# Kernel tuning notes

Measured on AMD Instinct MI355X. Metric: run time of the kernel, lower is better.

## Reference

```python
import jax, jax.numpy as jnp
import numpy as np

NUM_HEADS = 16
ROTARY_BASE = 10000.0


def _apply_rotary(x):
    # x: (B, S, H, D); GPT-NeoX style rotate-half over full head dim
    B, S, H, D = x.shape
    half = D // 2
    inv_freq = 1.0 / (ROTARY_BASE ** (jnp.arange(0, half, dtype=jnp.float32) / half))
    t = jnp.arange(S, dtype=jnp.float32)
    freqs = jnp.einsum('s,d->sd', t, inv_freq)          # (S, half)
    cos = jnp.cos(freqs)[None, :, None, :]               # (1, S, 1, half)
    sin = jnp.sin(freqs)[None, :, None, :]
    x1, x2 = x[..., :half], x[..., half:]
    return jnp.concatenate([x1 * cos - x2 * sin, x2 * cos + x1 * sin], axis=-1).astype(x.dtype)


def setup_inputs() -> dict:
    key = jax.random.key(0)
    k0, k1, k2 = jax.random.split(key, 3)
    B, S, E = 2, 2048, 2048
    x = jax.random.normal(k0, (B, S, E), dtype=jnp.float32)
    wqkv = jax.random.normal(k1, (3 * E, E), dtype=jnp.float32) * 0.02
    bqkv = jnp.zeros((3 * E,), dtype=jnp.float32)
    wout = jax.random.normal(k2, (E, E), dtype=jnp.float32) * 0.02
    bout = jnp.zeros((E,), dtype=jnp.float32)
    return {"x": x, "wqkv": wqkv, "bqkv": bqkv, "wout": wout, "bout": bout}


def reference(x, wqkv, bqkv, wout, bout):
    B, S, E = x.shape
    H = NUM_HEADS
    D = E // H
    # fused QKV projection: (B, S, 3, H, D)
    qkv = (jnp.einsum('bse,fe->bsf', x, wqkv) + bqkv).reshape(B, S, 3, H, D)
    q, k, v = qkv[:, :, 0], qkv[:, :, 1], qkv[:, :, 2]
    q = _apply_rotary(q)
    k = _apply_rotary(k)
    scale = 1.0 / jnp.sqrt(jnp.float32(D))
    scores = jnp.einsum('bthd,bshd->bhts', q, k) * scale  # (B, H, S, S)
    causal_mask = jnp.triu(jnp.full((S, S), -10000.0, dtype=scores.dtype), 1)
    attn = jax.nn.softmax(scores + causal_mask, axis=-1)
    ctx = jnp.einsum('bhts,bshd->bthd', attn, v).reshape(B, S, E)
    return jnp.einsum('bse,fe->bsf', ctx, wout) + bout
```

## Files before the change

### kernel.cpp

```cpp
#include <hip/hip_runtime.h>
#include <math.h>

#define BB 2
#define SS 2048
#define EE 2048
#define HH 16
#define DD 128
#define FF 6144

typedef __attribute__((ext_vector_type(8))) short short8;
typedef __attribute__((ext_vector_type(4))) float floatx4;

static __device__ __forceinline__ unsigned short f2bf(float x) {
  unsigned u = __float_as_uint(x);
  u += 0x7fffu + ((u >> 16) & 1u);
  return (unsigned short)(u >> 16);
}
static __device__ __forceinline__ float bf2f(unsigned short h) {
  return __uint_as_float((unsigned)h << 16);
}

#define GLOAD_LDS16(gp, lp)                                       \
  __builtin_amdgcn_global_load_lds(                               \
      (const __attribute__((address_space(1))) void*)(gp),        \
      (__attribute__((address_space(3))) void*)(lp), 16, 0, 0)

__global__ __launch_bounds__(256) void cast_f32_bf16(
    const float* __restrict__ in, unsigned short* __restrict__ out, int n4) {
  const int i = blockIdx.x * 256 + threadIdx.x;
  if (i >= n4) return;
  const float4 v = ((const float4*)in)[i];
  ushort4 o;
  o.x = f2bf(v.x); o.y = f2bf(v.y); o.z = f2bf(v.z); o.w = f2bf(v.w);
  ((ushort4*)out)[i] = o;
}

static __device__ __forceinline__ void store_out(float* p, float v) { *p = v; }
static __device__ __forceinline__ void store_out(unsigned short* p, float v) {
  *p = f2bf(v);
}

template <typename OutT>
__global__ __launch_bounds__(512, 2) void gemm_bf16_256x192(
    const unsigned short* __restrict__ A, const unsigned short* __restrict__ Bt,
    const float* __restrict__ bias, OutT* __restrict__ C,
    int M, int N, int K) {
  __shared__ __align__(16) unsigned short As[2][16384];
  __shared__ __align__(16) unsigned short Bs[2][12288];

  const int tid = threadIdx.x;
  const int w = tid >> 6;
  const int L = tid & 63;
  const int lane16 = L & 15;
  const int quad = L >> 4;
  const int wm = w >> 2;
  const int wn = w & 3;

  const int nby = M >> 8;
  const int q8 = gridDim.x >> 3;
  const int wg = (blockIdx.x & 7) * q8 + (blockIdx.x >> 3);
  const int by = wg % nby;
  const int bx = wg / nby;
  const int m0 = by << 8;
  const int n0 = bx * 192;

  const int lA = ((w >> 1) << 4) + (L >> 2);
  const int scol = ((w & 1) << 5) + (((L & 3) * 8) ^ ((L & 32) ? 16 : 0));
  unsigned aoff[4], boff[3];
#pragma unroll
  for (int j = 0; j < 4; ++j)
    aoff[j] = (unsigned)(m0 + j * 64 + lA) * (unsigned)K + scol;
#pragma unroll
  for (int j = 0; j < 3; ++j)
    boff[j] = (unsigned)(n0 + j * 64 + lA) * (unsigned)K + scol;
  const int ldst = w * 512;

  const int sq = (quad * 8) ^ ((lane16 & 8) << 1);
  const int rbase = lane16 * 32 + sq;

  floatx4 acc[8][3] = {};

  GLOAD_LDS16(A + aoff[0], &As[0][0 * 4096 + ldst]);
  GLOAD_LDS16(A + aoff[1], &As[0][1 * 4096 + ldst]);
  GLOAD_LDS16(A + aoff[2], &As[0][2 * 4096 + ldst]);
  GLOAD_LDS16(A + aoff[3], &As[0][3 * 4096 + ldst]);
  GLOAD_LDS16(Bt + boff[0], &Bs[0][0 * 4096 + ldst]);
  GLOAD_LDS16(Bt + boff[1], &Bs[0][1 * 4096 + ldst]);
  GLOAD_LDS16(Bt + boff[2], &Bs[0][2 * 4096 + ldst]);
  GLOAD_LDS16(Bt + boff[0] + 64, &Bs[1][0 * 4096 + ldst]);
  GLOAD_LDS16(Bt + boff[1] + 64, &Bs[1][1 * 4096 + ldst]);
  GLOAD_LDS16(Bt + boff[2] + 64, &Bs[1][2 * 4096 + ldst]);
  asm volatile("s_waitcnt vmcnt(3)" ::: "memory");
  __builtin_amdgcn_sched_barrier(0);
  __builtin_amdgcn_s_barrier();

  const int NT = K >> 6;
  short8 a[4][2], b[3][2];

  for (int t = 0; t < NT; ++t) {
    const int c = t & 1;
    const unsigned kn1 = (unsigned)(t + 1) << 6;
    const unsigned kn2 = (unsigned)(t + 2) << 6;
    const unsigned short* Ac = &As[c][0];
    const unsigned short* Bc = &Bs[c][0];

#pragma unroll
    for (int mi = 0; mi < 4; ++mi)
#pragma unroll
      for (int kk = 0; kk < 2; ++kk)
        a[mi][kk] = *(const short8*)(Ac + (wm * 2) * 4096 +
                                     ((mi * 2 + kk) * 512) + rbase);
#pragma unroll
    for (int ni = 0; ni < 3; ++ni) {
      const int f = wn * 3 + ni;
#pragma unroll
      for (int kk = 0; kk < 2; ++kk)
        b[ni][kk] = *(const short8*)(Bc + (f >> 2) * 4096 +
                                     (((f & 3) * 2 + kk) * 512) + rbase);
    }
    GLOAD_LDS16(A + aoff[0] + kn1, &As[c ^ 1][0 * 4096 + ldst]);
    GLOAD_LDS16(A + aoff[1] + kn1, &As[c ^ 1][1 * 4096 + ldst]);
    GLOAD_LDS16(A + aoff[2] + kn1, &As[c ^ 1][2 * 4096 + ldst]);
    GLOAD_LDS16(A + aoff[3] + kn1, &As[c ^ 1][3 * 4096 + ldst]);
    __builtin_amdgcn_s_setprio(1);
#pragma unroll
    for (int mi = 0; mi < 4; ++mi)
#pragma unroll
      for (int ni = 0; ni < 3; ++ni)
#pragma unroll
        for (int kk = 0; kk < 2; ++kk)
          acc[mi][ni] = __builtin_amdgcn_mfma_f32_16x16x32_bf16(
              a[mi][kk], b[ni][kk], acc[mi][ni], 0, 0, 0);
    __builtin_amdgcn_s_setprio(0);
    __builtin_amdgcn_sched_barrier(0);
    __builtin_amdgcn_s_barrier();

#pragma unroll
    for (int mi = 0; mi < 4; ++mi)
#pragma unroll
      for (int kk = 0; kk < 2; ++kk)
        a[mi][kk] = *(const short8*)(Ac + (wm * 2 + 1) * 4096 +
                                     ((mi * 2 + kk) * 512) + rbase);
    GLOAD_LDS16(Bt + boff[0] + kn2, &Bs[c][0 * 4096 + ldst]);
    GLOAD_LDS16(Bt + boff[1] + kn2, &Bs[c][1 * 4096 + ldst]);
    GLOAD_LDS16(Bt + boff[2] + kn2, &Bs[c][2 * 4096 + ldst]);
    __builtin_amdgcn_s_setprio(1);
#pragma unroll
    for (int mi = 0; mi < 4; ++mi)
#pragma unroll
      for (int ni = 0; ni < 3; ++ni)
#pragma unroll
        for (int kk = 0; kk < 2; ++kk)
          acc[4 + mi][ni] = __builtin_amdgcn_mfma_f32_16x16x32_bf16(
              a[mi][kk], b[ni][kk], acc[4 + mi][ni], 0, 0, 0);
    __builtin_amdgcn_s_setprio(0);
    asm volatile("s_waitcnt vmcnt(3)" ::: "memory");
    __builtin_amdgcn_sched_barrier(0);
    __builtin_amdgcn_s_barrier();
  }

#pragma unroll
  for (int ni = 0; ni < 3; ++ni) {
    const int col = n0 + wn * 48 + ni * 16 + lane16;
    const float bv = bias[col];
#pragma unroll
    for (int mi = 0; mi < 8; ++mi) {
      const int row = m0 + wm * 128 + mi * 16 + quad * 4;
#pragma unroll
      for (int r = 0; r < 4; ++r)
        store_out(&C[(size_t)(row + r) * N + col], acc[mi][ni][r] + bv);
    }
  }
}

template <typename OutT>
__global__ __launch_bounds__(512, 2) void gemm_bf16_256x128(
    const unsigned short* __restrict__ A, const unsigned short* __restrict__ Bt,
    const float* __restrict__ bias, OutT* __restrict__ C,
    int M, int N, int K) {
  __shared__ __align__(16) unsigned short As[2][16384];
  __shared__ __align__(16) unsigned short Bs[2][8192];

  const int tid = threadIdx.x;
  const int w = tid >> 6;
  const int L = tid & 63;
  const int lane16 = L & 15;
  const int quad = L >> 4;
  const int wm = w >> 2;
  const int wn = w & 3;

  const int nby = M >> 8;
  const int q8 = gridDim.x >> 3;
  const int wg = (blockIdx.x & 7) * q8 + (blockIdx.x >> 3);
  const int by = wg % nby;
  const int bx = wg / nby;
  const int m0 = by << 8;
  const int n0 = bx << 7;

  const int lA = ((w >> 1) << 4) + (L >> 2);
  const int scol = ((w & 1) << 5) + (((L & 3) * 8) ^ ((L & 32) ? 16 : 0));
  unsigned aoff[4], boff[2];
#pragma unroll
  for (int j = 0; j < 4; ++j)
    aoff[j] = (unsigned)(m0 + j * 64 + lA) * (unsigned)K + scol;
#pragma unroll
  for (int j = 0; j < 2; ++j)
    boff[j] = (unsigned)(n0 + j * 64 + lA) * (unsigned)K + scol;
  const int ldst = w * 512;

  const int sq = (quad * 8) ^ ((lane16 & 8) << 1);
  const int rbase = lane16 * 32 + sq;

  floatx4 acc[8][2] = {};

  GLOAD_LDS16(A + aoff[0], &As[0][0 * 4096 + ldst]);
  GLOAD_LDS16(A + aoff[1], &As[0][1 * 4096 + ldst]);
  GLOAD_LDS16(A + aoff[2], &As[0][2 * 4096 + ldst]);
  GLOAD_LDS16(A + aoff[3], &As[0][3 * 4096 + ldst]);
  GLOAD_LDS16(Bt + boff[0], &Bs[0][0 * 4096 + ldst]);
  GLOAD_LDS16(Bt + boff[1], &Bs[0][1 * 4096 + ldst]);
  GLOAD_LDS16(Bt + boff[0] + 64, &Bs[1][0 * 4096 + ldst]);
  GLOAD_LDS16(Bt + boff[1] + 64, &Bs[1][1 * 4096 + ldst]);
  asm volatile("s_waitcnt vmcnt(2)" ::: "memory");
  __builtin_amdgcn_sched_barrier(0);
  __builtin_amdgcn_s_barrier();

  const int NT = K >> 6;
  short8 a[4][2], b[2][2];

  for (int t = 0; t < NT; ++t) {
    const int c = t & 1;
    const unsigned kn1 = (unsigned)(t + 1) << 6;
    const unsigned kn2 = (unsigned)(t + 2) << 6;
    const unsigned short* Ac = &As[c][0];
    const unsigned short* Bc = &Bs[c][0];

#pragma unroll
    for (int mi = 0; mi < 4; ++mi)
#pragma unroll
      for (int kk = 0; kk < 2; ++kk)
        a[mi][kk] = *(const short8*)(Ac + (wm * 2) * 4096 +
                                     ((mi * 2 + kk) * 512) + rbase);
#pragma unroll
    for (int ni = 0; ni < 2; ++ni) {
      const int f = wn * 2 + ni;
#pragma unroll
      for (int kk = 0; kk < 2; ++kk)
        b[ni][kk] = *(const short8*)(Bc + (f >> 2) * 4096 +
                                     (((f & 3) * 2 + kk) * 512) + rbase);
    }
    GLOAD_LDS16(A + aoff[0] + kn1, &As[c ^ 1][0 * 4096 + ldst]);
    GLOAD_LDS16(A + aoff[1] + kn1, &As[c ^ 1][1 * 4096 + ldst]);
    GLOAD_LDS16(A + aoff[2] + kn1, &As[c ^ 1][2 * 4096 + ldst]);
    GLOAD_LDS16(A + aoff[3] + kn1, &As[c ^ 1][3 * 4096 + ldst]);
    __builtin_amdgcn_s_setprio(1);
#pragma unroll
    for (int mi = 0; mi < 4; ++mi)
#pragma unroll
      for (int ni = 0; ni < 2; ++ni)
#pragma unroll
        for (int kk = 0; kk < 2; ++kk)
          acc[mi][ni] = __builtin_amdgcn_mfma_f32_16x16x32_bf16(
              a[mi][kk], b[ni][kk], acc[mi][ni], 0, 0, 0);
    __builtin_amdgcn_s_setprio(0);
    __builtin_amdgcn_sched_barrier(0);
    __builtin_amdgcn_s_barrier();

#pragma unroll
    for (int mi = 0; mi < 4; ++mi)
#pragma unroll
      for (int kk = 0; kk < 2; ++kk)
        a[mi][kk] = *(const short8*)(Ac + (wm * 2 + 1) * 4096 +
                                     ((mi * 2 + kk) * 512) + rbase);
    GLOAD_LDS16(Bt + boff[0] + kn2, &Bs[c][0 * 4096 + ldst]);
    GLOAD_LDS16(Bt + boff[1] + kn2, &Bs[c][1 * 4096 + ldst]);
    __builtin_amdgcn_s_setprio(1);
#pragma unroll
    for (int mi = 0; mi < 4; ++mi)
#pragma unroll
      for (int ni = 0; ni < 2; ++ni)
#pragma unroll
        for (int kk = 0; kk < 2; ++kk)
          acc[4 + mi][ni] = __builtin_amdgcn_mfma_f32_16x16x32_bf16(
              a[mi][kk], b[ni][kk], acc[4 + mi][ni], 0, 0, 0);
    __builtin_amdgcn_s_setprio(0);
    asm volatile("s_waitcnt vmcnt(2)" ::: "memory");
    __builtin_amdgcn_sched_barrier(0);
    __builtin_amdgcn_s_barrier();
  }

#pragma unroll
  for (int ni = 0; ni < 2; ++ni) {
    const int col = n0 + wn * 32 + ni * 16 + lane16;
    const float bv = bias[col];
#pragma unroll
    for (int mi = 0; mi < 8; ++mi) {
      const int row = m0 + wm * 128 + mi * 16 + quad * 4;
#pragma unroll
      for (int r = 0; r < 4; ++r)
        store_out(&C[(size_t)(row + r) * N + col], acc[mi][ni][r] + bv);
    }
  }
}

__global__ __launch_bounds__(256) void rotary_kernel(unsigned short* __restrict__ qkv) {
  const int idx = blockIdx.x * blockDim.x + threadIdx.x;
  const int d = idx & 63;
  const int h = (idx >> 6) & (HH - 1);
  const int s = (idx >> 10) & (SS - 1);
  const int b = idx >> 21;

  const float inv_freq = __expf(-(float)d * 0.14391156509f);
  float sn, c;
  __sincosf((float)s * inv_freq, &sn, &c);

  const size_t base = ((size_t)b * SS + s) * FF + h * DD + d;
  unsigned short* q = qkv + base;
  unsigned short* k = qkv + base + EE;

  const float q1 = bf2f(q[0]), q2 = bf2f(q[64]);
  q[0]  = f2bf(q1 * c - q2 * sn);
  q[64] = f2bf(q2 * c + q1 * sn);
  const float k1 = bf2f(k[0]), k2 = bf2f(k[64]);
  k[0]  = f2bf(k1 * c - k2 * sn);
  k[64] = f2bf(k2 * c + k1 * sn);
}

__global__ __launch_bounds__(256) void transpose_v(
    const unsigned short* __restrict__ qkv, unsigned short* __restrict__ vt) {
  __shared__ unsigned short T[64][72];
  const int t = threadIdx.x;
  const int s0 = blockIdx.x * 64;
  const int d0 = blockIdx.y * 64;
  const int bh = blockIdx.z;
  const int b = bh >> 4, h = bh & 15;
  {
    const int r = t >> 2, c = (t & 3) * 16;
    const unsigned short* src =
        qkv + ((size_t)b * SS + s0 + r) * FF + 2 * EE + h * DD + d0 + c;
    const uint4 u0 = *(const uint4*)src;
    const uint4 u1 = *(const uint4*)(src + 8);
    *(uint4*)&T[r][c] = u0;
    *(uint4*)&T[r][c + 8] = u1;
  }
  __syncthreads();
  {
    const int rr = t >> 2, cc = (t & 3) * 16;
    unsigned short vals[16];
#pragma unroll
    for (int j = 0; j < 16; ++j) vals[j] = T[cc + j][rr];
    unsigned short* dst =
        vt + (size_t)bh * DD * SS + (size_t)(d0 + rr) * SS + s0 + cc;
    *(uint4*)dst = *(uint4*)&vals[0];
    *(uint4*)(dst + 8) = *(uint4*)&vals[8];
  }
}

#define ATQ 128
#define ATK 32
#define SPAD 40
#define NQT (SS / ATQ)

__global__ __launch_bounds__(512, 4) void attn_mfma(
    const unsigned short* __restrict__ qkv,
    const unsigned short* __restrict__ vt,
    unsigned short* __restrict__ ctx) {
  __shared__ __align__(16) unsigned short Ksh[2][ATK * DD];
  __shared__ __align__(16) unsigned short Vsh[2][DD * ATK];
  __shared__ __align__(16) unsigned short Ssh[ATQ][SPAD];

  const int tid = threadIdx.x;
  const int L = tid & 63;
  const int w = tid >> 6;
  const int lane16 = L & 15;
  const int quad = L >> 4;

  const int flat = blockIdx.x;
  const int bh_lin = flat & 31;
  const int qb = (NQT - 1) - (flat >> 5);
  const int b = bh_lin >> 4;
  const int h = bh_lin & 15;
  const int bh = b * HH + h;
  const float scale = 0.08838834764831845f;

  const int kkrow = tid >> 4;
  const int cgk = (tid & 15) ^ (kkrow & 15);
  const size_t koff =
      ((size_t)b * SS + kkrow) * FF + EE + h * DD + cgk * 8;
  const int drow = tid >> 2;
  const int cgv = (tid & 3) ^ (drow & 3);
  const size_t voff = (size_t)bh * DD * SS + (size_t)drow * SS + cgv * 8;
  const int dstKV = w * 512;

  const int q0 = qb * ATQ;

  short8 qf[4];
  {
    const int q = q0 + w * 16 + lane16;
    const unsigned short* qp =
        qkv + ((size_t)b * SS + q) * FF + h * DD + quad * 8;
#pragma unroll
    for (int dc = 0; dc < 4; ++dc) qf[dc] = *(const short8*)(qp + dc * 32);
  }

  floatx4 acc[8] = {};
  float m_i = -3.0e38f;
  float l_i = 0.0f;

  const int nkt = 4 * qb + 4;
  const int mykt = 4 * qb + (w >> 1);

  GLOAD_LDS16(qkv + koff, &Ksh[0][dstKV]);
  GLOAD_LDS16(vt + voff, &Vsh[0][dstKV]);

  for (int kt = 0; kt < nkt; ++kt) {
    const int cur = kt & 1;
    __syncthreads();
    if (kt + 1 < nkt) {
      const size_t ka = (size_t)(kt + 1) * ATK * FF;
      const int va = (kt + 1) * ATK;
      GLOAD_LDS16(qkv + koff + ka, &Ksh[cur ^ 1][dstKV]);
      GLOAD_LDS16(vt + voff + va, &Vsh[cur ^ 1][dstKV]);
    }
    if (kt > mykt) continue;
    const int k0 = kt * ATK;
    const unsigned short* Kc = Ksh[cur];
    const unsigned short* Vc = Vsh[cur];

    floatx4 st[2] = {};
    __builtin_amdgcn_s_setprio(1);
#pragma unroll
    for (int kkt = 0; kkt < 2; ++kkt) {
      const unsigned short* krow = Kc + (kkt * 16 + lane16) * 128;
#pragma unroll
      for (int dc = 0; dc < 4; ++dc) {
        const short8 kf =
            *(const short8*)(krow + ((dc * 4 + quad) ^ lane16) * 8);
        st[kkt] = __builtin_amdgcn_mfma_f32_16x16x32_bf16(
            kf, qf[dc], st[kkt], 0, 0, 0);
      }
    }
    __builtin_amdgcn_s_setprio(0);

    const bool needmask = (kt == mykt);
    const int q_glob = q0 + w * 16 + lane16;
#pragma unroll
    for (int kkt = 0; kkt < 2; ++kkt) {
      const int kkb = k0 + kkt * 16 + quad * 4;
#pragma unroll
      for (int r = 0; r < 4; ++r) {
        float v = st[kkt][r] * scale;
        if (needmask && (kkb + r) > q_glob) v = -3.0e38f;
        st[kkt][r] = v;
      }
    }

    {
      float tm = -3.0e38f;
#pragma unroll
      for (int kkt = 0; kkt < 2; ++kkt)
#pragma unroll
        for (int r = 0; r < 4; ++r) tm = fmaxf(tm, st[kkt][r]);
      tm = fmaxf(tm, __shfl_xor(tm, 16));
      tm = fmaxf(tm, __shfl_xor(tm, 32));

      const bool need = !__all(tm - m_i <= 8.0f);
      if (need) {
        const float mn = fmaxf(m_i, tm);
        const float alpha = __expf(m_i - mn);
        m_i = mn;
        l_i *= alpha;
#pragma unroll
        for (int dt = 0; dt < 8; ++dt)
#pragma unroll
          for (int r = 0; r < 4; ++r) acc[dt][r] *= alpha;
      }

      float rs = 0.0f;
#pragma unroll
      for (int kkt = 0; kkt < 2; ++kkt)
#pragma unroll
        for (int r = 0; r < 4; ++r) {
          const float p = __expf(st[kkt][r] - m_i);
          st[kkt][r] = p;
          rs += p;
        }
      rs += __shfl_xor(rs, 16);
      rs += __shfl_xor(rs, 32);
      l_i += rs;

#pragma unroll
      for (int kkt = 0; kkt < 2; ++kkt) {
        ushort4 pk;
        pk.x = f2bf(st[kkt][0]);
        pk.y = f2bf(st[kkt][1]);
        pk.z = f2bf(st[kkt][2]);
        pk.w = f2bf(st[kkt][3]);
        *(ushort4*)(&Ssh[w * 16 + lane16][kkt * 16 + quad * 4]) = pk;
      }
    }

    const short8 pa =
        *(const short8*)(&Ssh[w * 16 + lane16][quad * 8]);
    const int vpos = (quad ^ (lane16 & 3)) * 8;
    __builtin_amdgcn_s_setprio(1);
#pragma unroll
    for (int dt = 0; dt < 8; ++dt) {
      const short8 vf = *(const short8*)(Vc + (dt * 16 + lane16) * 32 + vpos);
      acc[dt] = __builtin_amdgcn_mfma_f32_16x16x32_bf16(
          vf, pa, acc[dt], 0, 0, 0);
    }
    __builtin_amdgcn_s_setprio(0);
  }

  {
    const float inv = 1.0f / l_i;
    const int q = q0 + w * 16 + lane16;
    unsigned short* op = ctx + ((size_t)b * SS + q) * EE + h * DD + quad * 4;
#pragma unroll
    for (int dt = 0; dt < 8; ++dt) {
      ushort4 o;
      o.x = f2bf(acc[dt][0] * inv);
      o.y = f2bf(acc[dt][1] * inv);
      o.z = f2bf(acc[dt][2] * inv);
      o.w = f2bf(acc[dt][3] * inv);
      *(ushort4*)(op + dt * 16) = o;
    }
  }
}

extern "C" void kernel_launch(void* const* d_in, const int* in_sizes, int n_in,
                              void* d_out, int out_size, void* d_ws,
                              size_t ws_size, hipStream_t stream) {
  const float* x    = (const float*)d_in[0];
  const float* wqkv = (const float*)d_in[1];
  const float* bqkv = (const float*)d_in[2];
  const float* wout = (const float*)d_in[3];
  const float* bout = (const float*)d_in[4];
  float* out = (float*)d_out;

  unsigned short* qkvb = (unsigned short*)d_ws;
  unsigned short* xb   = qkvb + (size_t)25165824;
  unsigned short* wqb  = xb + (size_t)8388608;
  unsigned short* ctxb = wqb + (size_t)12582912;
  unsigned short* wob  = ctxb + (size_t)8388608;
  unsigned short* vtb  = wob + (size_t)4194304;

  const int M = BB * SS;

  cast_f32_bf16<<<8192, 256, 0, stream>>>(x, xb, 2097152);
  cast_f32_bf16<<<12288, 256, 0, stream>>>(wqkv, wqb, 3145728);
  cast_f32_bf16<<<4096, 256, 0, stream>>>(wout, wob, 1048576);

  {
    gemm_bf16_256x192<unsigned short><<<dim3(512), 512, 0, stream>>>(
        xb, wqb, bqkv, qkvb, M, FF, EE);
  }
  {
    const int total = BB * SS * HH * 64;
    rotary_kernel<<<total / 256, 256, 0, stream>>>(qkvb);
  }
  {
    dim3 grid(SS / 64, DD / 64, BB * HH);
    transpose_v<<<grid, 256, 0, stream>>>(qkvb, vtb);
  }
  {
    attn_mfma<<<dim3(512), 512, 0, stream>>>(qkvb, vtb, ctxb);
  }
  {
    gemm_bf16_256x128<float><<<dim3(256), 512, 0, stream>>>(
        ctxb, wob, bout, out, M, EE, EE);
  }
}
```

Before: 398.3 us.

## Merge cast and rope/transpose launches; widen attention tiles to 64 keys, 2 q-subtiles

The three f32-to-bf16 casts become one launch, and the rotary and V-transpose kernels merge into one launch split by block index, removing launch gaps. The attention kernel drops to 256 threads, each wave handling two 16-row query subtiles against 64-key tiles. This reuses each K/V fragment load for two MFMAs and halves the number of loop iterations and barriers, with an XOR-swizzled P buffer in shared memory. In exchange it raises register pressure (two accumulator sets) and uses more shared memory per block, which may lower occupancy.

```diff
diff --git a/kernel.cpp b/kernel.cpp
--- a/kernel.cpp
+++ b/kernel.cpp
@@ -25,14 +25,25 @@
       (const __attribute__((address_space(1))) void*)(gp),        \
       (__attribute__((address_space(3))) void*)(lp), 16, 0, 0)
 
-__global__ __launch_bounds__(256) void cast_f32_bf16(
-    const float* __restrict__ in, unsigned short* __restrict__ out, int n4) {
+__global__ __launch_bounds__(256) void cast_all(
+    const float* __restrict__ x, const float* __restrict__ wqkv,
+    const float* __restrict__ wout, unsigned short* __restrict__ xb,
+    unsigned short* __restrict__ wqb, unsigned short* __restrict__ wob) {
   const int i = blockIdx.x * 256 + threadIdx.x;
-  if (i >= n4) return;
-  const float4 v = ((const float4*)in)[i];
+  const float* src;
+  unsigned short* dst;
+  int off;
+  if (i < 2097152) {
+    src = x; dst = xb; off = i;
+  } else if (i < 5242880) {
+    src = wqkv; dst = wqb; off = i - 2097152;
+  } else {
+    src = wout; dst = wob; off = i - 5242880;
+  }
+  const float4 v = ((const float4*)src)[off];
   ushort4 o;
   o.x = f2bf(v.x); o.y = f2bf(v.y); o.z = f2bf(v.z); o.w = f2bf(v.w);
-  ((ushort4*)out)[i] = o;
+  ((ushort4*)dst)[off] = o;
 }
 
 static __device__ __forceinline__ void store_out(float* p, float v) { *p = v; }
@@ -303,71 +314,71 @@
   }
 }
 
-__global__ __launch_bounds__(256) void rotary_kernel(unsigned short* __restrict__ qkv) {
-  const int idx = blockIdx.x * blockDim.x + threadIdx.x;
-  const int d = idx & 63;
-  const int h = (idx >> 6) & (HH - 1);
-  const int s = (idx >> 10) & (SS - 1);
-  const int b = idx >> 21;
-
-  const float inv_freq = __expf(-(float)d * 0.14391156509f);
-  float sn, c;
-  __sincosf((float)s * inv_freq, &sn, &c);
-
-  const size_t base = ((size_t)b * SS + s) * FF + h * DD + d;
-  unsigned short* q = qkv + base;
-  unsigned short* k = qkv + base + EE;
-
-  const float q1 = bf2f(q[0]), q2 = bf2f(q[64]);
-  q[0]  = f2bf(q1 * c - q2 * sn);
-  q[64] = f2bf(q2 * c + q1 * sn);
-  const float k1 = bf2f(k[0]), k2 = bf2f(k[64]);
-  k[0]  = f2bf(k1 * c - k2 * sn);
-  k[64] = f2bf(k2 * c + k1 * sn);
-}
-
-__global__ __launch_bounds__(256) void transpose_v(
-    const unsigned short* __restrict__ qkv, unsigned short* __restrict__ vt) {
-  __shared__ unsigned short T[64][72];
-  const int t = threadIdx.x;
-  const int s0 = blockIdx.x * 64;
-  const int d0 = blockIdx.y * 64;
-  const int bh = blockIdx.z;
-  const int b = bh >> 4, h = bh & 15;
-  {
-    const int r = t >> 2, c = (t & 3) * 16;
-    const unsigned short* src =
-        qkv + ((size_t)b * SS + s0 + r) * FF + 2 * EE + h * DD + d0 + c;
-    const uint4 u0 = *(const uint4*)src;
-    const uint4 u1 = *(const uint4*)(src + 8);
-    *(uint4*)&T[r][c] = u0;
-    *(uint4*)&T[r][c + 8] = u1;
-  }
-  __syncthreads();
-  {
-    const int rr = t >> 2, cc = (t & 3) * 16;
-    unsigned short vals[16];
-#pragma unroll
-    for (int j = 0; j < 16; ++j) vals[j] = T[cc + j][rr];
-    unsigned short* dst =
-        vt + (size_t)bh * DD * SS + (size_t)(d0 + rr) * SS + s0 + cc;
-    *(uint4*)dst = *(uint4*)&vals[0];
-    *(uint4*)(dst + 8) = *(uint4*)&vals[8];
+__global__ __launch_bounds__(256) void rope_transpose(
+    unsigned short* __restrict__ qkv, unsigned short* __restrict__ vt) {
+  if (blockIdx.x < 16384) {
+    const int idx = blockIdx.x * 256 + threadIdx.x;
+    const int d = idx & 63;
+    const int h = (idx >> 6) & (HH - 1);
+    const int s = (idx >> 10) & (SS - 1);
+    const int b = idx >> 21;
+
+    const float inv_freq = __expf(-(float)d * 0.14391156509f);
+    float sn, c;
+    __sincosf((float)s * inv_freq, &sn, &c);
+
+    const size_t base = ((size_t)b * SS + s) * FF + h * DD + d;
+    unsigned short* q = qkv + base;
+    unsigned short* k = qkv + base + EE;
+
+    const float q1 = bf2f(q[0]), q2 = bf2f(q[64]);
+    q[0]  = f2bf(q1 * c - q2 * sn);
+    q[64] = f2bf(q2 * c + q1 * sn);
+    const float k1 = bf2f(k[0]), k2 = bf2f(k[64]);
+    k[0]  = f2bf(k1 * c - k2 * sn);
+    k[64] = f2bf(k2 * c + k1 * sn);
+  } else {
+    __shared__ unsigned short T[64][72];
+    const int idx = blockIdx.x - 16384;
+    const int t = threadIdx.x;
+    const int s0 = (idx & 31) * 64;
+    const int d0 = ((idx >> 5) & 1) * 64;
+    const int bh = idx >> 6;
+    const int b = bh >> 4, h = bh & 15;
+    {
+      const int r = t >> 2, c = (t & 3) * 16;
+      const unsigned short* src =
+          qkv + ((size_t)b * SS + s0 + r) * FF + 2 * EE + h * DD + d0 + c;
+      const uint4 u0 = *(const uint4*)src;
+      const uint4 u1 = *(const uint4*)(src + 8);
+      *(uint4*)&T[r][c] = u0;
+      *(uint4*)&T[r][c + 8] = u1;
+    }
+    __syncthreads();
+    {
+      const int rr = t >> 2, cc = (t & 3) * 16;
+      unsigned short vals[16];
+#pragma unroll
+      for (int j = 0; j < 16; ++j) vals[j] = T[cc + j][rr];
+      unsigned short* dst =
+          vt + (size_t)bh * DD * SS + (size_t)(d0 + rr) * SS + s0 + cc;
+      *(uint4*)dst = *(uint4*)&vals[0];
+      *(uint4*)(dst + 8) = *(uint4*)&vals[8];
+    }
   }
 }
 
 #define ATQ 128
-#define ATK 32
-#define SPAD 40
+#define ATK 64
 #define NQT (SS / ATQ)
 
-__global__ __launch_bounds__(512, 4) void attn_mfma(
+__global__ __launch_bounds__(256, 2) void attn_mfma(
     const unsigned short* __restrict__ qkv,
     const unsigned short* __restrict__ vt,
     unsigned short* __restrict__ ctx) {
   __shared__ __align__(16) unsigned short Ksh[2][ATK * DD];
   __shared__ __align__(16) unsigned short Vsh[2][DD * ATK];
-  __shared__ __align__(16) unsigned short Ssh[ATQ][SPAD];
+  __shared__ __align__(16) unsigned short Ssh[ATQ][64];
 
   const int tid = threadIdx.x;
   const int L = tid & 63;
@@ -383,35 +394,44 @@
   const int bh = b * HH + h;
   const float scale = 0.08838834764831845f;
 
-  const int kkrow = tid >> 4;
-  const int cgk = (tid & 15) ^ (kkrow & 15);
-  const size_t koff =
-      ((size_t)b * SS + kkrow) * FF + EE + h * DD + cgk * 8;
-  const int drow = tid >> 2;
-  const int cgv = (tid & 3) ^ (drow & 3);
-  const size_t voff = (size_t)bh * DD * SS + (size_t)drow * SS + cgv * 8;
-  const int dstKV = w * 512;
+  size_t koff[4], voff[4];
+#pragma unroll
+  for (int j = 0; j < 4; ++j) {
+    const int ik = j * 256 + tid;
+    const int kk = ik >> 4;
+    const int ock = (ik & 15) ^ (kk & 15);
+    koff[j] = ((size_t)b * SS + kk) * FF + EE + h * DD + ock * 8;
+    const int d = ik >> 3;
+    const int ocv = (ik & 7) ^ (d & 7);
+    voff[j] = (size_t)bh * DD * SS + (size_t)d * SS + ocv * 8;
+  }
+  const int dstb = w * 512;
 
   const int q0 = qb * ATQ;
 
-  short8 qf[4];
-  {
-    const int q = q0 + w * 16 + lane16;
+  short8 qf[2][4];
+#pragma unroll
+  for (int mi = 0; mi < 2; ++mi) {
+    const int q = q0 + w * 32 + mi * 16 + lane16;
     const unsigned short* qp =
         qkv + ((size_t)b * SS + q) * FF + h * DD + quad * 8;
 #pragma unroll
-    for (int dc = 0; dc < 4; ++dc) qf[dc] = *(const short8*)(qp + dc * 32);
-  }
-
-  floatx4 acc[8] = {};
-  float m_i = -3.0e38f;
-  float l_i = 0.0f;
-
-  const int nkt = 4 * qb + 4;
-  const int mykt = 4 * qb + (w >> 1);
-
-  GLOAD_LDS16(qkv + koff, &Ksh[0][dstKV]);
-  GLOAD_LDS16(vt + voff, &Vsh[0][dstKV]);
+    for (int dc = 0; dc < 4; ++dc)
+      qf[mi][dc] = *(const short8*)(qp + dc * 32);
+  }
+
+  floatx4 acc[8][2] = {};
+  float m_i[2] = {-3.0e38f, -3.0e38f};
+  float l_i[2] = {0.0f, 0.0f};
+
+  const int nkt = 2 * qb + 2;
+  const int mykt = 2 * qb + (w >> 1);
+
+#pragma unroll
+  for (int j = 0; j < 4; ++j) {
+    GLOAD_LDS16(qkv + koff[j], &Ksh[0][j * 2048 + dstb]);
+    GLOAD_LDS16(vt + voff[j], &Vsh[0][j * 2048 + dstb]);
+  }
 
   for (int kt = 0; kt < nkt; ++kt) {
     const int cur = kt & 1;
@@ -419,111 +439,137 @@
     if (kt + 1 < nkt) {
       const size_t ka = (size_t)(kt + 1) * ATK * FF;
       const int va = (kt + 1) * ATK;
-      GLOAD_LDS16(qkv + koff + ka, &Ksh[cur ^ 1][dstKV]);
-      GLOAD_LDS16(vt + voff + va, &Vsh[cur ^ 1][dstKV]);
+#pragma unroll
+      for (int j = 0; j < 4; ++j) {
+        GLOAD_LDS16(qkv + koff[j] + ka, &Ksh[cur ^ 1][j * 2048 + dstb]);
+        GLOAD_LDS16(vt + voff[j] + va, &Vsh[cur ^ 1][j * 2048 + dstb]);
+      }
     }
     if (kt > mykt) continue;
     const int k0 = kt * ATK;
     const unsigned short* Kc = Ksh[cur];
     const unsigned short* Vc = Vsh[cur];
 
-    floatx4 st[2] = {};
+    floatx4 st[4][2] = {};
     __builtin_amdgcn_s_setprio(1);
 #pragma unroll
-    for (int kkt = 0; kkt < 2; ++kkt) {
+    for (int kkt = 0; kkt < 4; ++kkt) {
       const unsigned short* krow = Kc + (kkt * 16 + lane16) * 128;
 #pragma unroll
       for (int dc = 0; dc < 4; ++dc) {
         const short8 kf =
             *(const short8*)(krow + ((dc * 4 + quad) ^ lane16) * 8);
-        st[kkt] = __builtin_amdgcn_mfma_f32_16x16x32_bf16(
-            kf, qf[dc], st[kkt], 0, 0, 0);
+#pragma unroll
+        for (int mi = 0; mi < 2; ++mi)
+          st[kkt][mi] = __builtin_amdgcn_mfma_f32_16x16x32_bf16(
+              kf, qf[mi][dc], st[kkt][mi], 0, 0, 0);
       }
     }
     __builtin_amdgcn_s_setprio(0);
 
     const bool needmask = (kt == mykt);
-    const int q_glob = q0 + w * 16 + lane16;
-#pragma unroll
-    for (int kkt = 0; kkt < 2; ++kkt) {
-      const int kkb = k0 + kkt * 16 + quad * 4;
-#pragma unroll
-      for (int r = 0; r < 4; ++r) {
-        float v = st[kkt][r] * scale;
-        if (needmask && (kkb + r) > q_glob) v = -3.0e38f;
-        st[kkt][r] = v;
+#pragma unroll
+    for (int mi = 0; mi < 2; ++mi) {
+      const int q_glob = q0 + w * 32 + mi * 16 + lane16;
+#pragma unroll
+      for (int kkt = 0; kkt < 4; ++kkt) {
+        const int kkb = k0 + kkt * 16 + quad * 4;
+#pragma unroll
+        for (int r = 0; r < 4; ++r) {
+          float v = st[kkt][mi][r] * scale;
+          if (needmask && (kkb + r) > q_glob) v = -3.0e38f;
+          st[kkt][mi][r] = v;
+        }
       }
     }
 
-    {
+#pragma unroll
+    for (int mi = 0; mi < 2; ++mi) {
       float tm = -3.0e38f;
 #pragma unroll
-      for (int kkt = 0; kkt < 2; ++kkt)
-#pragma unroll
-        for (int r = 0; r < 4; ++r) tm = fmaxf(tm, st[kkt][r]);
+      for (int kkt = 0; kkt < 4; ++kkt)
+#pragma unroll
+        for (int r = 0; r < 4; ++r) tm = fmaxf(tm, st[kkt][mi][r]);
       tm = fmaxf(tm, __shfl_xor(tm, 16));
       tm = fmaxf(tm, __shfl_xor(tm, 32));
 
-      const bool need = !__all(tm - m_i <= 8.0f);
+      const bool need = !__all(tm - m_i[mi] <= 8.0f);
       if (need) {
-        const float mn = fmaxf(m_i, tm);
-        const float alpha = __expf(m_i - mn);
-        m_i = mn;
-        l_i *= alpha;
+        const float mn = fmaxf(m_i[mi], tm);
+        const float alpha = __expf(m_i[mi] - mn);
+        m_i[mi] = mn;
+        l_i[mi] *= alpha;
 #pragma unroll
         for (int dt = 0; dt < 8; ++dt)
 #pragma unroll
-          for (int r = 0; r < 4; ++r) acc[dt][r] *= alpha;
+          for (int r = 0; r < 4; ++r) acc[dt][mi][r] *= alpha;
       }
 
       float rs = 0.0f;
 #pragma unroll
-      for (int kkt = 0; kkt < 2; ++kkt)
+      for (int kkt = 0; kkt < 4; ++kkt)
 #pragma unroll
         for (int r = 0; r < 4; ++r) {
-          const float p = __expf(st[kkt][r] - m_i);
-          st[kkt][r] = p;
+          const float p = __expf(st[kkt][mi][r] - m_i[mi]);
+          st[kkt][mi][r] = p;
           rs += p;
         }
       rs += __shfl_xor(rs, 16);
       rs += __shfl_xor(rs, 32);
-      l_i += rs;
-
-#pragma unroll
-      for (int kkt = 0; kkt < 2; ++kkt) {
+      l_i[mi] += rs;
+
+      const int row = w * 32 + mi * 16 + lane16;
+      const int sw = 2 * (lane16 & 7);
+#pragma unroll
+      for (int kkt = 0; kkt < 4; ++kkt) {
         ushort4 pk;
-        pk.x = f2bf(st[kkt][0]);
-        pk.y = f2bf(st[kkt][1]);
-        pk.z = f2bf(st[kkt][2]);
-        pk.w = f2bf(st[kkt][3]);
-        *(ushort4*)(&Ssh[w * 16 + lane16][kkt * 16 + quad * 4]) = pk;
+        pk.x = f2bf(st[kkt][mi][0]);
+        pk.y = f2bf(st[kkt][mi][1]);
+        pk.z = f2bf(st[kkt][mi][2]);
+        pk.w = f2bf(st[kkt][mi][3]);
+        *(ushort4*)(&Ssh[row][((kkt * 4 + quad) ^ sw) * 4]) = pk;
       }
     }
 
-    const short8 pa =
-        *(const short8*)(&Ssh[w * 16 + lane16][quad * 8]);
-    const int vpos = (quad ^ (lane16 & 3)) * 8;
+    short8 pa[2][2];
+#pragma unroll
+    for (int mi = 0; mi < 2; ++mi) {
+      const int row = w * 32 + mi * 16 + lane16;
+      const int sw = 2 * (lane16 & 7);
+#pragma unroll
+      for (int ks = 0; ks < 2; ++ks)
+        pa[mi][ks] =
+            *(const short8*)(&Ssh[row][((ks * 8 + quad * 2) ^ sw) * 4]);
+    }
     __builtin_amdgcn_s_setprio(1);
 #pragma unroll
     for (int dt = 0; dt < 8; ++dt) {
-      const short8 vf = *(const short8*)(Vc + (dt * 16 + lane16) * 32 + vpos);
-      acc[dt] = __builtin_amdgcn_mfma_f32_16x16x32_bf16(
-          vf, pa, acc[dt], 0, 0, 0);
+      const unsigned short* vrow = Vc + (dt * 16 + lane16) * 64;
+#pragma unroll
+      for (int ks = 0; ks < 2; ++ks) {
+        const short8 vf =
+            *(const short8*)(vrow + (((ks * 4 + quad) ^ (lane16 & 7)) * 8));
+#pragma unroll
+        for (int mi = 0; mi < 2; ++mi)
+          acc[dt][mi] = __builtin_amdgcn_mfma_f32_16x16x32_bf16(
+              vf, pa[mi][ks], acc[dt][mi], 0, 0, 0);
+      }
     }
     __builtin_amdgcn_s_setprio(0);
   }
 
-  {
-    const float inv = 1.0f / l_i;
-    const int q = q0 + w * 16 + lane16;
+#pragma unroll
+  for (int mi = 0; mi < 2; ++mi) {
+    const float inv = 1.0f / l_i[mi];
+    const int q = q0 + w * 32 + mi * 16 + lane16;
     unsigned short* op = ctx + ((size_t)b * SS + q) * EE + h * DD + quad * 4;
 #pragma unroll
     for (int dt = 0; dt < 8; ++dt) {
       ushort4 o;
-      o.x = f2bf(acc[dt][0] * inv);
-      o.y = f2bf(acc[dt][1] * inv);
-      o.z = f2bf(acc[dt][2] * inv);
-      o.w = f2bf(acc[dt][3] * inv);
+      o.x = f2bf(acc[dt][mi][0] * inv);
+      o.y = f2bf(acc[dt][mi][1] * inv);
+      o.z = f2bf(acc[dt][mi][2] * inv);
+      o.w = f2bf(acc[dt][mi][3] * inv);
       *(ushort4*)(op + dt * 16) = o;
     }
   }
@@ -548,24 +594,17 @@
 
   const int M = BB * SS;
 
-  cast_f32_bf16<<<8192, 256, 0, stream>>>(x, xb, 2097152);
-  cast_f32_bf16<<<12288, 256, 0, stream>>>(wqkv, wqb, 3145728);
-  cast_f32_bf16<<<4096, 256, 0, stream>>>(wout, wob, 1048576);
+  cast_all<<<24576, 256, 0, stream>>>(x, wqkv, wout, xb, wqb, wob);
 
   {
     gemm_bf16_256x192<unsigned short><<<dim3(512), 512, 0, stream>>>(
         xb, wqb, bqkv, qkvb, M, FF, EE);
   }
   {
-    const int total = BB * SS * HH * 64;
-    rotary_kernel<<<total / 256, 256, 0, stream>>>(qkvb);
+    rope_transpose<<<18432, 256, 0, stream>>>(qkvb, vtb);
   }
   {
-    dim3 grid(SS / 64, DD / 64, BB * HH);
-    transpose_v<<<grid, 256, 0, stream>>>(qkvb, vtb);
-  }
-  {
-    attn_mfma<<<dim3(512), 512, 0, stream>>>(qkvb, vtb, ctxb);
+    attn_mfma<<<dim3(512), 256, 0, stream>>>(qkvb, vtb, ctxb);
   }
   {
     gemm_bf16_256x128<float><<<dim3(256), 512, 0, stream>>>(
```

Result: no change. 391.6 us (-1.7%).
